# Kernel optimization log

Measured on AMD Instinct MI355X. Metric: run time of the kernel, lower is better.

The kernel has to match this reference:

```python
import jax, jax.numpy as jnp
import numpy as np


def setup_inputs() -> dict:
    key = jax.random.key(0)
    k1, k2, k3 = jax.random.split(key, 3)
    B, N, K, F, H = 4, 50000, 10, 128, 16
    x = jax.random.normal(k1, (B, N, K, F), dtype=jnp.float32)
    # xavier-like scales for learned params
    W = jax.random.normal(k2, (F, 4 * H), dtype=jnp.float32) * (1.0 / np.sqrt(F))
    a = jax.random.normal(k3, (4, H), dtype=jnp.float32) * 0.5
    return {"x": x, "W": W, "a": a}


def reference(x, W, a):
    # x: [B, N, K, F]; W: [F, 4H] (head-major blocks of 4); a: [4, H]
    B, N, K, F = x.shape
    H = a.shape[1]
    Wr = W.reshape(F, H, 4)                              # per-head projection
    hw = jnp.einsum('bnkf,fhd->bnkhd', x, Wr)            # [B,N,K,H,4]
    logits = jnp.einsum('bnkhd,dh->bnkh', hw, a)         # [B,N,K,H]
    attn = jax.nn.softmax(logits, axis=2)                # softmax over K neighbors
    out = jnp.einsum('bnkh,bnkhd->bnhd', attn, hw)       # [B,N,H,4]
    out = jax.nn.leaky_relu(out, negative_slope=0.2)
    out = out.reshape(B, N, H * 4)                       # concat over heads
    return out.transpose(0, 2, 1)                        # [B, 4H, N]
```

## Files before the change

kernel.cpp:

```cpp
#include <hip/hip_runtime.h>

typedef short bf16x8 __attribute__((ext_vector_type(8)));
typedef float f32x4 __attribute__((ext_vector_type(4)));

constexpr int Bc = 4;
constexpr int Nc = 50000;
constexpr int Kc = 10;
constexpr int Fc = 128;
constexpr int Hc = 16;
constexpr int Cc = 64;
constexpr int NODES = Bc * Nc;
constexpr int NPB = 8;
constexpr int ROWS = NPB * Kc;
constexpr int MT = ROWS / 16;
constexpr int BLK = 256;

constexpr int LDS_BYTES = 23936;
constexpr int OL_OFF = 21760;

__device__ __forceinline__ unsigned short f2bf(float f) {
    unsigned u = __builtin_bit_cast(unsigned, f);
    return (unsigned short)((u + 0x7fffu + ((u >> 16) & 1u)) >> 16);
}

__global__ __launch_bounds__(256)
void prep_w(const float* __restrict__ W, unsigned short* __restrict__ wt) {
    const int dst = blockIdx.x * 256 + threadIdx.x;
    const int j  = dst & 7;
    const int kc = (dst >> 3) & 3;
    const int l  = (dst >> 5) & 63;
    const int w  = dst >> 11;
    const int c  = w * 16 + (l & 15);
    const int f  = kc * 32 + (l >> 4) * 8 + j;
    wt[dst] = f2bf(W[f * 64 + c]);
}

__global__ __launch_bounds__(BLK, 6)
void gat_kernel(const float* __restrict__ x,
                const unsigned short* __restrict__ wt_ws,
                const float* __restrict__ a,
                float* __restrict__ out)
{
    __shared__ __align__(16) char smem[LDS_BYTES];

    const int t  = threadIdx.x;
    const int w  = t >> 6;
    const int l  = t & 63;
    const int lr = l & 15;
    const int lk = l >> 4;

    bf16x8 bfrag[4];
    {
        const bf16x8* wp = reinterpret_cast<const bf16x8*>(wt_ws + w * 2048 + l * 32);
#pragma unroll
        for (int kc = 0; kc < 4; ++kc) bfrag[kc] = wp[kc];
    }

    {
        const float* xg = x + (size_t)blockIdx.x * (ROWS * Fc);
#pragma unroll
        for (int i = 0; i < 5; ++i) {
            const int e0 = i * 2048 + t * 8;
            const float4 v0 = *reinterpret_cast<const float4*>(xg + e0);
            const float4 v1 = *reinterpret_cast<const float4*>(xg + e0 + 4);
            const int row = i * 16 + (t >> 4);
            const int byt = ((t & 15) * 16) ^ ((row & 7) << 4);
            uint4 p;
            p.x = (unsigned)f2bf(v0.x) | ((unsigned)f2bf(v0.y) << 16);
            p.y = (unsigned)f2bf(v0.z) | ((unsigned)f2bf(v0.w) << 16);
            p.z = (unsigned)f2bf(v1.x) | ((unsigned)f2bf(v1.y) << 16);
            p.w = (unsigned)f2bf(v1.z) | ((unsigned)f2bf(v1.w) << 16);
            *reinterpret_cast<uint4*>(smem + row * 256 + byt) = p;
        }
    }
    __syncthreads();

    f32x4 acc[MT];
#pragma unroll
    for (int m = 0; m < MT; ++m) acc[m] = (f32x4){0.f, 0.f, 0.f, 0.f};

#pragma unroll
    for (int m = 0; m < MT; ++m) {
        const int row = m * 16 + lr;
        const char* xrow = smem + row * 256;
        const int sw = (row & 7) << 4;
#pragma unroll
        for (int kc = 0; kc < 4; ++kc) {
            const bf16x8 af = *reinterpret_cast<const bf16x8*>(xrow + ((kc * 64 + lk * 16) ^ sw));
            acc[m] = __builtin_amdgcn_mfma_f32_16x16x32_bf16(af, bfrag[kc], acc[m], 0, 0, 0);
        }
    }
    __syncthreads();

    {
        float* hw = reinterpret_cast<float*>(smem);
        const int col = w * 16 + lr;
#pragma unroll
        for (int m = 0; m < MT; ++m) {
            const int rbase = m * 16 + lk * 4;
#pragma unroll
            for (int r = 0; r < 4; ++r)
                hw[(rbase + r) * 68 + col] = acc[m][r];
        }
    }
    __syncthreads();

    const float* hw = reinterpret_cast<const float*>(smem);
    float* ol = reinterpret_cast<float*>(smem + OL_OFF);
    if (t < NPB * Hc) {
        const int h  = t & 15;
        const int ln = t >> 4;
        const float ar0 = a[0 * Hc + h];
        const float ar1 = a[1 * Hc + h];
        const float ar2 = a[2 * Hc + h];
        const float ar3 = a[3 * Hc + h];

        float4 hv[Kc];
        float  lg[Kc];
        float  mx = -1e30f;
#pragma unroll
        for (int k = 0; k < Kc; ++k) {
            hv[k] = *reinterpret_cast<const float4*>(hw + (ln * Kc + k) * 68 + h * 4);
            lg[k] = fmaf(hv[k].x, ar0, fmaf(hv[k].y, ar1, fmaf(hv[k].z, ar2, hv[k].w * ar3)));
            mx = fmaxf(mx, lg[k]);
        }
        float lsum = 0.f, o0 = 0.f, o1 = 0.f, o2 = 0.f, o3 = 0.f;
#pragma unroll
        for (int k = 0; k < Kc; ++k) {
            const float p = __expf(lg[k] - mx);
            lsum += p;
            o0 = fmaf(p, hv[k].x, o0);
            o1 = fmaf(p, hv[k].y, o1);
            o2 = fmaf(p, hv[k].z, o2);
            o3 = fmaf(p, hv[k].w, o3);
        }
        const float inv = 1.f / lsum;
        o0 *= inv; o1 *= inv; o2 *= inv; o3 *= inv;
        o0 = fmaxf(o0, 0.2f * o0);
        o1 = fmaxf(o1, 0.2f * o1);
        o2 = fmaxf(o2, 0.2f * o2);
        o3 = fmaxf(o3, 0.2f * o3);
        *reinterpret_cast<float4*>(ol + ln * 68 + h * 4) = make_float4(o0, o1, o2, o3);
    }
    __syncthreads();

    if (t < 128) {
        const int c  = t >> 1;
        const int nq = t & 1;
        const int nb = blockIdx.x * NPB;
        const int b  = nb / Nc;
        const int n0 = nb - b * Nc;
        float4 v;
        v.x = ol[(nq * 4 + 0) * 68 + c];
        v.y = ol[(nq * 4 + 1) * 68 + c];
        v.z = ol[(nq * 4 + 2) * 68 + c];
        v.w = ol[(nq * 4 + 3) * 68 + c];
        *reinterpret_cast<float4*>(out + ((size_t)b * Cc + c) * Nc + n0 + nq * 4) = v;
    }
}

extern "C" void kernel_launch(void* const* d_in, const int* in_sizes, int n_in,
                              void* d_out, int out_size, void* d_ws, size_t ws_size,
                              hipStream_t stream) {
    const float* x = (const float*)d_in[0];
    const float* W = (const float*)d_in[1];
    const float* a = (const float*)d_in[2];
    float* out = (float*)d_out;
    unsigned short* wt = (unsigned short*)d_ws;

    prep_w<<<32, 256, 0, stream>>>(W, wt);
    gat_kernel<<<NODES / NPB, BLK, 0, stream>>>(x, wt, a, out);
}
```

Measured before the change: 235.9 us.

## Make GAT kernel persistent with register prefetch of the next node tile

Turns the one-tile-per-block kernel into a persistent kernel with a fixed grid of 1024 blocks that stride over node tiles. While the current tile is in MFMA, softmax and store, each block holds the next tile's x values in registers, so global loads overlap compute. It also hoists the attention-vector loads out of the loop, replaces __syncthreads with an LDS-only wait plus barrier, and lowers the occupancy hint from 6 to 4. The cost is higher register pressure and fewer resident blocks per CU, which could reduce the memory parallelism available for this bandwidth-bound kernel.

```diff
diff --git a/kernel.cpp b/kernel.cpp
--- a/kernel.cpp
+++ b/kernel.cpp
@@ -14,6 +14,8 @@
 constexpr int ROWS = NPB * Kc;
 constexpr int MT = ROWS / 16;
 constexpr int BLK = 256;
+constexpr int NTILES = NODES / NPB;
+constexpr int NBLK = 1024;
 
 constexpr int LDS_BYTES = 23936;
 constexpr int OL_OFF = 21760;
@@ -21,6 +23,13 @@
 __device__ __forceinline__ unsigned short f2bf(float f) {
     unsigned u = __builtin_bit_cast(unsigned, f);
     return (unsigned short)((u + 0x7fffu + ((u >> 16) & 1u)) >> 16);
+}
+
+__device__ __forceinline__ void bar_lds() {
+    asm volatile("s_waitcnt lgkmcnt(0)" ::: "memory");
+    __builtin_amdgcn_sched_barrier(0);
+    __builtin_amdgcn_s_barrier();
+    __builtin_amdgcn_sched_barrier(0);
 }
 
 __global__ __launch_bounds__(256)
@@ -35,7 +44,7 @@
     wt[dst] = f2bf(W[f * 64 + c]);
 }
 
-__global__ __launch_bounds__(BLK, 6)
+__global__ __launch_bounds__(BLK, 4)
 void gat_kernel(const float* __restrict__ x,
                 const unsigned short* __restrict__ wt_ws,
                 const float* __restrict__ a,
@@ -56,13 +65,27 @@
         for (int kc = 0; kc < 4; ++kc) bfrag[kc] = wp[kc];
     }
 
+    const float ar0 = a[0 * Hc + (t & 15)];
+    const float ar1 = a[1 * Hc + (t & 15)];
+    const float ar2 = a[2 * Hc + (t & 15)];
+    const float ar3 = a[3 * Hc + (t & 15)];
+
+    int tile = blockIdx.x;
+    float4 st[10];
     {
-        const float* xg = x + (size_t)blockIdx.x * (ROWS * Fc);
+        const float* xg = x + (size_t)tile * (ROWS * Fc);
 #pragma unroll
         for (int i = 0; i < 5; ++i) {
-            const int e0 = i * 2048 + t * 8;
-            const float4 v0 = *reinterpret_cast<const float4*>(xg + e0);
-            const float4 v1 = *reinterpret_cast<const float4*>(xg + e0 + 4);
+            st[2 * i]     = *reinterpret_cast<const float4*>(xg + i * 2048 + t * 8);
+            st[2 * i + 1] = *reinterpret_cast<const float4*>(xg + i * 2048 + t * 8 + 4);
+        }
+    }
+
+    for (;;) {
+#pragma unroll
+        for (int i = 0; i < 5; ++i) {
+            const float4 v0 = st[2 * i];
+            const float4 v1 = st[2 * i + 1];
             const int row = i * 16 + (t >> 4);
             const int byt = ((t & 15) * 16) ^ ((row & 7) << 4);
             uint4 p;
@@ -72,90 +95,99 @@
             p.w = (unsigned)f2bf(v1.z) | ((unsigned)f2bf(v1.w) << 16);
             *reinterpret_cast<uint4*>(smem + row * 256 + byt) = p;
         }
-    }
-    __syncthreads();
-
-    f32x4 acc[MT];
-#pragma unroll
-    for (int m = 0; m < MT; ++m) acc[m] = (f32x4){0.f, 0.f, 0.f, 0.f};
-
-#pragma unroll
-    for (int m = 0; m < MT; ++m) {
-        const int row = m * 16 + lr;
-        const char* xrow = smem + row * 256;
-        const int sw = (row & 7) << 4;
-#pragma unroll
-        for (int kc = 0; kc < 4; ++kc) {
-            const bf16x8 af = *reinterpret_cast<const bf16x8*>(xrow + ((kc * 64 + lk * 16) ^ sw));
-            acc[m] = __builtin_amdgcn_mfma_f32_16x16x32_bf16(af, bfrag[kc], acc[m], 0, 0, 0);
-        }
-    }
-    __syncthreads();
-
-    {
-        float* hw = reinterpret_cast<float*>(smem);
-        const int col = w * 16 + lr;
+        bar_lds();
+
+        const int ntile = tile + NBLK;
+        if (ntile < NTILES) {
+            const float* xg = x + (size_t)ntile * (ROWS * Fc);
+#pragma unroll
+            for (int i = 0; i < 5; ++i) {
+                st[2 * i]     = *reinterpret_cast<const float4*>(xg + i * 2048 + t * 8);
+                st[2 * i + 1] = *reinterpret_cast<const float4*>(xg + i * 2048 + t * 8 + 4);
+            }
+        }
+
+        f32x4 acc[MT];
+#pragma unroll
+        for (int m = 0; m < MT; ++m) acc[m] = (f32x4){0.f, 0.f, 0.f, 0.f};
 #pragma unroll
         for (int m = 0; m < MT; ++m) {
-            const int rbase = m * 16 + lk * 4;
-#pragma unroll
-            for (int r = 0; r < 4; ++r)
-                hw[(rbase + r) * 68 + col] = acc[m][r];
-        }
-    }
-    __syncthreads();
-
-    const float* hw = reinterpret_cast<const float*>(smem);
-    float* ol = reinterpret_cast<float*>(smem + OL_OFF);
-    if (t < NPB * Hc) {
-        const int h  = t & 15;
-        const int ln = t >> 4;
-        const float ar0 = a[0 * Hc + h];
-        const float ar1 = a[1 * Hc + h];
-        const float ar2 = a[2 * Hc + h];
-        const float ar3 = a[3 * Hc + h];
-
-        float4 hv[Kc];
-        float  lg[Kc];
-        float  mx = -1e30f;
-#pragma unroll
-        for (int k = 0; k < Kc; ++k) {
-            hv[k] = *reinterpret_cast<const float4*>(hw + (ln * Kc + k) * 68 + h * 4);
-            lg[k] = fmaf(hv[k].x, ar0, fmaf(hv[k].y, ar1, fmaf(hv[k].z, ar2, hv[k].w * ar3)));
-            mx = fmaxf(mx, lg[k]);
-        }
-        float lsum = 0.f, o0 = 0.f, o1 = 0.f, o2 = 0.f, o3 = 0.f;
-#pragma unroll
-        for (int k = 0; k < Kc; ++k) {
-            const float p = __expf(lg[k] - mx);
-            lsum += p;
-            o0 = fmaf(p, hv[k].x, o0);
-            o1 = fmaf(p, hv[k].y, o1);
-            o2 = fmaf(p, hv[k].z, o2);
-            o3 = fmaf(p, hv[k].w, o3);
-        }
-        const float inv = 1.f / lsum;
-        o0 *= inv; o1 *= inv; o2 *= inv; o3 *= inv;
-        o0 = fmaxf(o0, 0.2f * o0);
-        o1 = fmaxf(o1, 0.2f * o1);
-        o2 = fmaxf(o2, 0.2f * o2);
-        o3 = fmaxf(o3, 0.2f * o3);
-        *reinterpret_cast<float4*>(ol + ln * 68 + h * 4) = make_float4(o0, o1, o2, o3);
-    }
-    __syncthreads();
-
-    if (t < 128) {
-        const int c  = t >> 1;
-        const int nq = t & 1;
-        const int nb = blockIdx.x * NPB;
-        const int b  = nb / Nc;
-        const int n0 = nb - b * Nc;
-        float4 v;
-        v.x = ol[(nq * 4 + 0) * 68 + c];
-        v.y = ol[(nq * 4 + 1) * 68 + c];
-        v.z = ol[(nq * 4 + 2) * 68 + c];
-        v.w = ol[(nq * 4 + 3) * 68 + c];
-        *reinterpret_cast<float4*>(out + ((size_t)b * Cc + c) * Nc + n0 + nq * 4) = v;
+            const int row = m * 16 + lr;
+            const char* xrow = smem + row * 256;
+            const int sw = (row & 7) << 4;
+#pragma unroll
+            for (int kc = 0; kc < 4; ++kc) {
+                const bf16x8 af = *reinterpret_cast<const bf16x8*>(xrow + ((kc * 64 + lk * 16) ^ sw));
+                acc[m] = __builtin_amdgcn_mfma_f32_16x16x32_bf16(af, bfrag[kc], acc[m], 0, 0, 0);
+            }
+        }
+        bar_lds();
+
+        {
+            float* hw = reinterpret_cast<float*>(smem);
+            const int col = w * 16 + lr;
+#pragma unroll
+            for (int m = 0; m < MT; ++m) {
+                const int rbase = m * 16 + lk * 4;
+#pragma unroll
+                for (int r = 0; r < 4; ++r)
+                    hw[(rbase + r) * 68 + col] = acc[m][r];
+            }
+        }
+        bar_lds();
+
+        {
+            const float* hw = reinterpret_cast<const float*>(smem);
+            float* ol = reinterpret_cast<float*>(smem + OL_OFF);
+            if (t < NPB * Hc) {
+                const int ln = t >> 4;
+                float4 hv[Kc];
+                float  lg[Kc];
+                float  mx = -1e30f;
+#pragma unroll
+                for (int k = 0; k < Kc; ++k) {
+                    hv[k] = *reinterpret_cast<const float4*>(hw + (ln * Kc + k) * 68 + (t & 15) * 4);
+                    lg[k] = fmaf(hv[k].x, ar0, fmaf(hv[k].y, ar1, fmaf(hv[k].z, ar2, hv[k].w * ar3)));
+                    mx = fmaxf(mx, lg[k]);
+                }
+                float lsum = 0.f, o0 = 0.f, o1 = 0.f, o2 = 0.f, o3 = 0.f;
+#pragma unroll
+                for (int k = 0; k < Kc; ++k) {
+                    const float p = __expf(lg[k] - mx);
+                    lsum += p;
+                    o0 = fmaf(p, hv[k].x, o0);
+                    o1 = fmaf(p, hv[k].y, o1);
+                    o2 = fmaf(p, hv[k].z, o2);
+                    o3 = fmaf(p, hv[k].w, o3);
+                }
+                const float inv = 1.f / lsum;
+                o0 *= inv; o1 *= inv; o2 *= inv; o3 *= inv;
+                o0 = fmaxf(o0, 0.2f * o0);
+                o1 = fmaxf(o1, 0.2f * o1);
+                o2 = fmaxf(o2, 0.2f * o2);
+                o3 = fmaxf(o3, 0.2f * o3);
+                *reinterpret_cast<float4*>(ol + ln * 68 + (t & 15) * 4) = make_float4(o0, o1, o2, o3);
+            }
+        }
+        bar_lds();
+
+        if (t < 128) {
+            const float* ol = reinterpret_cast<const float*>(smem + OL_OFF);
+            const int c  = t >> 1;
+            const int nq = t & 1;
+            const int nb = tile * NPB;
+            const int b  = nb / Nc;
+            const int n0 = nb - b * Nc;
+            float4 v;
+            v.x = ol[(nq * 4 + 0) * 68 + c];
+            v.y = ol[(nq * 4 + 1) * 68 + c];
+            v.z = ol[(nq * 4 + 2) * 68 + c];
+            v.w = ol[(nq * 4 + 3) * 68 + c];
+            *reinterpret_cast<float4*>(out + ((size_t)b * Cc + c) * Nc + n0 + nq * 4) = v;
+        }
+
+        tile = ntile;
+        if (tile >= NTILES) break;
     }
 }
 
@@ -169,5 +201,5 @@
     unsigned short* wt = (unsigned short*)d_ws;
 
     prep_w<<<32, 256, 0, stream>>>(W, wt);
-    gat_kernel<<<NODES / NPB, BLK, 0, stream>>>(x, wt, a, out);
-}
+    gat_kernel<<<NBLK, BLK, 0, stream>>>(x, wt, a, out);
+}
```

New measurement: 251.5 us. 1.07x slower.
